# Kernel optimization log

Hardware: AMD Instinct MI355X
Metric: run time of the kernel (lower is better)

Reference implementation:

```python
import jax, jax.numpy as jnp
import numpy as np

B, T, F, U = 64, 512, 256, 1024


def setup_inputs() -> dict:
    key = jax.random.key(0)
    k1, k2, k3, k4 = jax.random.split(key, 4)
    x = jax.random.normal(k1, (B, T, F), dtype=jnp.float32)
    hidden = jnp.zeros((B, U), dtype=jnp.float32)  # initialize_hidden_state()
    # Keras GRU params (reset_after=True, the default): kernel [F,3U], recurrent
    # kernel [U,3U], and two bias vectors (input-side and recurrent-side) [2,3U].
    glorot_k = float(np.sqrt(2.0 / (F + 3 * U)))
    glorot_r = float(np.sqrt(2.0 / (U + 3 * U)))
    kernel = jax.random.normal(k2, (F, 3 * U), dtype=jnp.float32) * glorot_k
    recurrent_kernel = jax.random.normal(k3, (U, 3 * U), dtype=jnp.float32) * glorot_r
    bias = jax.random.normal(k4, (2, 3 * U), dtype=jnp.float32) * 0.02
    return {"x": x, "hidden": hidden, "kernel": kernel,
            "recurrent_kernel": recurrent_kernel, "bias": bias}


def reference(x, hidden, kernel, recurrent_kernel, bias):
    # Keras GRU, reset_after=True, activation=tanh, recurrent_activation=sigmoid.
    # Dropout/recurrent_dropout are inference no-ops (eval mode).
    b_in, b_rec = bias[0], bias[1]
    # Precompute the input projection for all timesteps: [B,T,3U]
    xp = jnp.einsum('btf,fg->btg', x, kernel) + b_in

    def step(h, xt):
        rec = h @ recurrent_kernel + b_rec            # [B,3U]
        xz, xr, xh = jnp.split(xt, 3, axis=-1)
        rz, rr, rh = jnp.split(rec, 3, axis=-1)
        z = jax.nn.sigmoid(xz + rz)                    # update gate
        r = jax.nn.sigmoid(xr + rr)                    # reset gate
        hh = jnp.tanh(xh + r * rh)                     # candidate (reset_after)
        h_new = z * h + (1.0 - z) * hh
        return h_new, h_new

    state, outs = jax.lax.scan(step, hidden, jnp.swapaxes(xp, 0, 1))
    output = jnp.swapaxes(outs, 0, 1)                  # [B,T,U]
    return output, state
```

## Files before the change

### kernel.cpp

```cpp
#include <hip/hip_runtime.h>

#define T_STEPS 512
#define B_ROWS  64
#define F_DIM   256
#define U_DIM   1024
#define G3      3072
#define PACC_BYTES (2 * 12 * 64 * 16)
#define LDS_BYTES (PACC_BYTES + 512)

#define NSLOT  5
#define TILE_B 512
#define GRP_B  (64 * TILE_B)
#define SLOT_B (4 * GRP_B)
#define SENT   0x7FC17FC1u

typedef __bf16 bf16x8 __attribute__((ext_vector_type(8)));
typedef float  f32x4  __attribute__((ext_vector_type(4)));
typedef unsigned int u32x2 __attribute__((ext_vector_type(2)));
typedef unsigned int u32x4 __attribute__((ext_vector_type(4)));

__device__ __forceinline__ float sigmoidf_(float v) {
    return 1.f / (1.f + __expf(-v));
}
__device__ __forceinline__ float tanhf_(float v) {
    float e2 = __expf(2.f * v);
    return 1.f - 2.f / (e2 + 1.f);
}

__global__ __launch_bounds__(256) void transpose_cvt_kernel(
    const float* __restrict__ src, __bf16* __restrict__ dst, int Kdim)
{
    __shared__ float tile[32][33];
    const int n0 = blockIdx.x * 32;
    const int k0 = blockIdx.y * 32;
    const int j  = threadIdx.x & 31;
    const int i0 = threadIdx.x >> 5;
#pragma unroll
    for (int s = 0; s < 4; ++s) {
        int i = i0 * 4 + s;
        tile[i][j] = src[(size_t)(k0 + i) * G3 + n0 + j];
    }
    __syncthreads();
#pragma unroll
    for (int s = 0; s < 4; ++s) {
        int i = i0 * 4 + s;
        dst[(size_t)(n0 + i) * Kdim + k0 + j] = (__bf16)tile[j][i];
    }
}

__global__ __launch_bounds__(256) void init_kernel(
    const float* __restrict__ hidden, char* __restrict__ rot)
{
    const int i = blockIdx.x * 256 + threadIdx.x;
    const int row = i >> 10, u = i & 1023;
    const int rt = row >> 4, rl = row & 15, c = u >> 4, ul = u & 15;
    *(__bf16*)(rot + rt * GRP_B + c * TILE_B + ((rl << 4) + ul) * 2) =
        (__bf16)hidden[i];
    unsigned* s = (unsigned*)(rot + SLOT_B);
    s[2 * i]     = SENT;
    s[2 * i + 1] = SENT;
}

__global__ __launch_bounds__(256, 1) void gru_persistent(
    const float* __restrict__ x,
    const float* __restrict__ hidden,
    const float* __restrict__ bias,
    const float* __restrict__ kern,
    const __bf16* __restrict__ Rt,
    char* __restrict__ rot,
    float* __restrict__ out)
{
    extern __shared__ char lds_raw[];
    float*  pacc  = (float*)lds_raw;
    __bf16* hpack = (__bf16*)(lds_raw + PACC_BYTES);

    const int tid  = threadIdx.x;
    const int lane = tid & 63;
    const int wv   = tid >> 6;
    const int rc   = lane & 15;
    const int kg   = lane >> 4;
    const int bid  = blockIdx.x;
    const int c    = bid & 63;
    const int rt   = bid >> 6;
    const int u    = (c << 4) + rc;
    const int row0 = rt << 4;

    if (wv == 0) __builtin_amdgcn_s_setprio(1);

    const int gu0 = u;
    const int gu1 = U_DIM + u;
    const int gu2 = 2 * U_DIM + u;
    const int xk0 = wv << 6;

    bf16x8 whz[8], whr[8], whh[8];
#pragma unroll
    for (int ki = 0; ki < 8; ++ki) {
        const int col = (wv << 8) + (ki << 5) + (kg << 3);
        whz[ki] = *(const bf16x8*)(Rt + (size_t)gu0 * U_DIM + col);
        whr[ki] = *(const bf16x8*)(Rt + (size_t)gu1 * U_DIM + col);
        whh[ki] = *(const bf16x8*)(Rt + (size_t)gu2 * U_DIM + col);
    }
    bf16x8 wxz[2], wxr[2], wxh[2];
#pragma unroll
    for (int fx = 0; fx < 2; ++fx) {
#pragma unroll
        for (int e = 0; e < 8; ++e) {
            const int k = xk0 + fx * 32 + (kg << 3) + e;
            wxz[fx][e] = (__bf16)kern[(size_t)k * G3 + gu0];
            wxr[fx][e] = (__bf16)kern[(size_t)k * G3 + gu1];
            wxh[fx][e] = (__bf16)kern[(size_t)k * G3 + gu2];
        }
    }

    float hprev[4];
#pragma unroll
    for (int j = 0; j < 4; ++j)
        hprev[j] = hidden[(size_t)(row0 + (kg << 2) + j) * U_DIM + u];

    const float bz_ = bias[u]             + bias[G3 + u];
    const float br_ = bias[U_DIM + u]     + bias[G3 + U_DIM + u];
    const float bhx = bias[2 * U_DIM + u];
    const float bhr = bias[G3 + 2 * U_DIM + u];

    const float* xbase = x + (size_t)(row0 + rc) * (T_STEPS * F_DIM)
                           + xk0 + (kg << 3);

    const int grp_b = rt * GRP_B;
    const int lan_b = (wv << 13) + ((kg >> 1) << 9) + (rc << 5) + ((kg & 1) << 4);
    const int my_b  = grp_b + c * TILE_B + (lane << 3);

    int slot_r = 0, slot_w = 1, slot_p = 3;
    const u32x2 sentv = { SENT, SENT };

    for (int t = 0; t < T_STEPS; ++t) {
        f32x4 accZ  = {0.f, 0.f, 0.f, 0.f};
        f32x4 accR  = {0.f, 0.f, 0.f, 0.f};
        f32x4 accHX = {0.f, 0.f, 0.f, 0.f};
        f32x4 accHR = {0.f, 0.f, 0.f, 0.f};
        const int p = t & 1;

        const char* hb = rot + slot_r * SLOT_B + grp_b + lan_b;
        bf16x8 hfrag[8];
#define HL(ki, m, lit)                                                         \
        asm volatile("global_load_dwordx4 %0, %1, off offset:" lit " sc0 sc1"  \
                     : "=v"(hfrag[ki]) : "v"(hb + (m) * 4096) : "memory");
#define HLOADS()                                                               \
        HL(0,0,"0") HL(1,0,"1024") HL(2,0,"2048") HL(3,0,"3072")               \
        HL(4,1,"0") HL(5,1,"1024") HL(6,1,"2048") HL(7,1,"3072")
        HLOADS()

        const float* ap = xbase + t * F_DIM;
#pragma unroll
        for (int fx = 0; fx < 2; ++fx) {
            const float4 a0 = *(const float4*)(ap + fx * 32);
            const float4 a1 = *(const float4*)(ap + fx * 32 + 4);
            bf16x8 af;
            af[0] = (__bf16)a0.x; af[1] = (__bf16)a0.y;
            af[2] = (__bf16)a0.z; af[3] = (__bf16)a0.w;
            af[4] = (__bf16)a1.x; af[5] = (__bf16)a1.y;
            af[6] = (__bf16)a1.z; af[7] = (__bf16)a1.w;
            accZ  = __builtin_amdgcn_mfma_f32_16x16x32_bf16(af, wxz[fx], accZ,  0, 0, 0);
            accR  = __builtin_amdgcn_mfma_f32_16x16x32_bf16(af, wxr[fx], accR,  0, 0, 0);
            accHX = __builtin_amdgcn_mfma_f32_16x16x32_bf16(af, wxh[fx], accHX, 0, 0, 0);
        }

        if (wv == 0 && t > 0) {
#pragma unroll
            for (int j = 0; j < 4; ++j) {
                const int row = row0 + (kg << 2) + j;
                out[((size_t)row * T_STEPS + (t - 1)) * U_DIM + u] = hprev[j];
            }
        }

        for (;;) {
            asm volatile("s_waitcnt vmcnt(0)" ::: "memory");
            __builtin_amdgcn_sched_barrier(0);
            int ok = 1;
#pragma unroll
            for (int ki = 0; ki < 8; ++ki) {
                const u32x4 w = __builtin_bit_cast(u32x4, hfrag[ki]);
                ok &= (w[0] != SENT) & (w[2] != SENT);
            }
            if (__all(ok)) break;
            HLOADS()
        }
#undef HLOADS
#undef HL

#pragma unroll
        for (int ki = 0; ki < 8; ++ki) {
            const bf16x8 af = hfrag[ki];
            accZ  = __builtin_amdgcn_mfma_f32_16x16x32_bf16(af, whz[ki], accZ,  0, 0, 0);
            accR  = __builtin_amdgcn_mfma_f32_16x16x32_bf16(af, whr[ki], accR,  0, 0, 0);
            accHR = __builtin_amdgcn_mfma_f32_16x16x32_bf16(af, whh[ki], accHR, 0, 0, 0);
        }

        if (wv != 0) {
            const int w1 = wv - 1;
            *(f32x4*)&pacc[(((p * 12) + 0 * 3 + w1) * 64 + lane) * 4] = accZ;
            *(f32x4*)&pacc[(((p * 12) + 1 * 3 + w1) * 64 + lane) * 4] = accR;
            *(f32x4*)&pacc[(((p * 12) + 2 * 3 + w1) * 64 + lane) * 4] = accHX;
            *(f32x4*)&pacc[(((p * 12) + 3 * 3 + w1) * 64 + lane) * 4] = accHR;
        }
        __syncthreads();

        if (wv == 0) {
#pragma unroll
            for (int w1 = 0; w1 < 3; ++w1) {
                accZ  += *(const f32x4*)&pacc[(((p * 12) + 0 * 3 + w1) * 64 + lane) * 4];
                accR  += *(const f32x4*)&pacc[(((p * 12) + 1 * 3 + w1) * 64 + lane) * 4];
                accHX += *(const f32x4*)&pacc[(((p * 12) + 2 * 3 + w1) * 64 + lane) * 4];
                accHR += *(const f32x4*)&pacc[(((p * 12) + 3 * 3 + w1) * 64 + lane) * 4];
            }
#pragma unroll
            for (int j = 0; j < 4; ++j) {
                const float z  = sigmoidf_(accZ[j] + bz_);
                const float r  = sigmoidf_(accR[j] + br_);
                const float hh = tanhf_(accHX[j] + bhx + r * (accHR[j] + bhr));
                hprev[j] = z * hprev[j] + (1.f - z) * hh;
            }
#pragma unroll
            for (int j = 0; j < 4; ++j)
                hpack[(((kg << 2) + j) << 4) + rc] = (__bf16)hprev[j];
            const u32x2 hv = *(const u32x2*)(hpack + ((lane >> 2) << 4) + ((lane & 3) << 2));
            asm volatile("global_store_dwordx2 %0, %1, off sc0 sc1"
                         :: "v"(rot + slot_w * SLOT_B + my_b), "v"(hv) : "memory");
            asm volatile("global_store_dwordx2 %0, %1, off sc0 sc1"
                         :: "v"(rot + slot_p * SLOT_B + my_b), "v"(sentv) : "memory");
        }

        if (++slot_r == NSLOT) slot_r = 0;
        if (++slot_w == NSLOT) slot_w = 0;
        if (++slot_p == NSLOT) slot_p = 0;
    }

    if (wv == 0) {
#pragma unroll
        for (int j = 0; j < 4; ++j) {
            const int row = row0 + (kg << 2) + j;
            out[((size_t)row * T_STEPS + (T_STEPS - 1)) * U_DIM + u] = hprev[j];
            out[(size_t)B_ROWS * T_STEPS * U_DIM + (size_t)row * U_DIM + u] = hprev[j];
        }
    }
}

extern "C" void kernel_launch(void* const* d_in, const int* in_sizes, int n_in,
                              void* d_out, int out_size, void* d_ws, size_t ws_size,
                              hipStream_t stream)
{
    const float* x      = (const float*)d_in[0];
    const float* hidden = (const float*)d_in[1];
    const float* kernel = (const float*)d_in[2];
    const float* rker   = (const float*)d_in[3];
    const float* bias   = (const float*)d_in[4];
    float* out = (float*)d_out;

    const size_t rt_el = (size_t)G3 * U_DIM;
    __bf16* Rt = (__bf16*)d_ws;
    char* rot  = (char*)(Rt + rt_el);

    hipLaunchKernelGGL(transpose_cvt_kernel, dim3(G3 / 32, U_DIM / 32), dim3(256),
                       0, stream, rker, Rt, U_DIM);
    hipLaunchKernelGGL(init_kernel, dim3(256), dim3(256), 0, stream, hidden, rot);

    void* kx = (void*)&x;  void* kh = (void*)&hidden; void* kb = (void*)&bias;
    void* kk = (void*)&kernel; void* kR = (void*)&Rt;
    void* kr = (void*)&rot; void* ko = (void*)&out;
    void* args[7] = { kx, kh, kb, kk, kR, kr, ko };

    auto kfn = gru_persistent;
    (void)hipFuncSetAttribute((const void*)kfn,
                              hipFuncAttributeMaxDynamicSharedMemorySize, LDS_BYTES);
    hipError_t ce = hipLaunchCooperativeKernel(kfn, dim3(256), dim3(256), args,
                                               LDS_BYTES, stream);
    if (ce != hipSuccess) {
        hipLaunchKernelGGL(gru_persistent, dim3(256), dim3(256), LDS_BYTES, stream,
                           x, hidden, bias, kernel, Rt, rot, out);
    }
}
```

Before: 1.388 ms.

## Offload input projection from critical wave and move sentinel store to another wave

Wave 0, which runs the gate math and publishes h, no longer does any input-projection MFMAs. Those chunks are redistributed to waves 1-3 as 3, 3 and 2 K-chunks. The sentinel-clear store moves from wave 0 to wave 3, and wave 0 uses a partial vmcnt wait that skips the output stores it just issued. This shortens the per-step serial path on wave 0, the one that gates cross-block propagation, at the cost of uneven work across the other waves.

```diff
diff --git a/kernel.cpp b/kernel.cpp
--- a/kernel.cpp
+++ b/kernel.cpp
@@ -90,7 +90,6 @@
     const int gu0 = u;
     const int gu1 = U_DIM + u;
     const int gu2 = 2 * U_DIM + u;
-    const int xk0 = wv << 6;
 
     bf16x8 whz[8], whr[8], whh[8];
 #pragma unroll
@@ -100,30 +99,35 @@
         whr[ki] = *(const bf16x8*)(Rt + (size_t)gu1 * U_DIM + col);
         whh[ki] = *(const bf16x8*)(Rt + (size_t)gu2 * U_DIM + col);
     }
-    bf16x8 wxz[2], wxr[2], wxh[2];
-#pragma unroll
-    for (int fx = 0; fx < 2; ++fx) {
-#pragma unroll
-        for (int e = 0; e < 8; ++e) {
-            const int k = xk0 + fx * 32 + (kg << 3) + e;
-            wxz[fx][e] = (__bf16)kern[(size_t)k * G3 + gu0];
-            wxr[fx][e] = (__bf16)kern[(size_t)k * G3 + gu1];
-            wxh[fx][e] = (__bf16)kern[(size_t)k * G3 + gu2];
-        }
-    }
-
-    float hprev[4];
-#pragma unroll
-    for (int j = 0; j < 4; ++j)
-        hprev[j] = hidden[(size_t)(row0 + (kg << 2) + j) * U_DIM + u];
-
+
+    const int xnck = (wv == 1 || wv == 2) ? 3 : (wv == 3 ? 2 : 0);
+    const int xoff = (wv == 2) ? 96 : (wv == 3 ? 192 : 0);
+    bf16x8 wxz[3], wxr[3], wxh[3];
+#pragma unroll
+    for (int ci = 0; ci < 3; ++ci) {
+        if (ci < xnck) {
+#pragma unroll
+            for (int e = 0; e < 8; ++e) {
+                const int k = xoff + ci * 32 + (kg << 3) + e;
+                wxz[ci][e] = (__bf16)kern[(size_t)k * G3 + gu0];
+                wxr[ci][e] = (__bf16)kern[(size_t)k * G3 + gu1];
+                wxh[ci][e] = (__bf16)kern[(size_t)k * G3 + gu2];
+            }
+        }
+    }
+
+    float hprev[4] = {0.f, 0.f, 0.f, 0.f};
+    if (wv == 0) {
+#pragma unroll
+        for (int j = 0; j < 4; ++j)
+            hprev[j] = hidden[(size_t)(row0 + (kg << 2) + j) * U_DIM + u];
+    }
     const float bz_ = bias[u]             + bias[G3 + u];
     const float br_ = bias[U_DIM + u]     + bias[G3 + U_DIM + u];
     const float bhx = bias[2 * U_DIM + u];
     const float bhr = bias[G3 + 2 * U_DIM + u];
 
-    const float* xbase = x + (size_t)(row0 + rc) * (T_STEPS * F_DIM)
-                           + xk0 + (kg << 3);
+    const float* xbase = x + (size_t)(row0 + rc) * (T_STEPS * F_DIM) + (kg << 3);
 
     const int grp_b = rt * GRP_B;
     const int lan_b = (wv << 13) + ((kg >> 1) << 9) + (rc << 5) + ((kg & 1) << 4);
@@ -149,40 +153,62 @@
         HL(4,1,"0") HL(5,1,"1024") HL(6,1,"2048") HL(7,1,"3072")
         HLOADS()
 
-        const float* ap = xbase + t * F_DIM;
-#pragma unroll
-        for (int fx = 0; fx < 2; ++fx) {
-            const float4 a0 = *(const float4*)(ap + fx * 32);
-            const float4 a1 = *(const float4*)(ap + fx * 32 + 4);
-            bf16x8 af;
-            af[0] = (__bf16)a0.x; af[1] = (__bf16)a0.y;
-            af[2] = (__bf16)a0.z; af[3] = (__bf16)a0.w;
-            af[4] = (__bf16)a1.x; af[5] = (__bf16)a1.y;
-            af[6] = (__bf16)a1.z; af[7] = (__bf16)a1.w;
-            accZ  = __builtin_amdgcn_mfma_f32_16x16x32_bf16(af, wxz[fx], accZ,  0, 0, 0);
-            accR  = __builtin_amdgcn_mfma_f32_16x16x32_bf16(af, wxr[fx], accR,  0, 0, 0);
-            accHX = __builtin_amdgcn_mfma_f32_16x16x32_bf16(af, wxh[fx], accHX, 0, 0, 0);
-        }
-
-        if (wv == 0 && t > 0) {
-#pragma unroll
-            for (int j = 0; j < 4; ++j) {
-                const int row = row0 + (kg << 2) + j;
-                out[((size_t)row * T_STEPS + (t - 1)) * U_DIM + u] = hprev[j];
-            }
-        }
-
-        for (;;) {
-            asm volatile("s_waitcnt vmcnt(0)" ::: "memory");
-            __builtin_amdgcn_sched_barrier(0);
-            int ok = 1;
-#pragma unroll
-            for (int ki = 0; ki < 8; ++ki) {
-                const u32x4 w = __builtin_bit_cast(u32x4, hfrag[ki]);
-                ok &= (w[0] != SENT) & (w[2] != SENT);
-            }
-            if (__all(ok)) break;
-            HLOADS()
+        if (wv == 0) {
+            if (t > 0) {
+#pragma unroll
+                for (int j = 0; j < 4; ++j) {
+                    const int row = row0 + (kg << 2) + j;
+                    out[((size_t)row * T_STEPS + (t - 1)) * U_DIM + u] = hprev[j];
+                }
+            }
+            bool first = (t > 0);
+            for (;;) {
+                if (first) {
+                    asm volatile("s_waitcnt vmcnt(4)" ::: "memory");
+                    first = false;
+                } else {
+                    asm volatile("s_waitcnt vmcnt(0)" ::: "memory");
+                }
+                __builtin_amdgcn_sched_barrier(0);
+                int ok = 1;
+#pragma unroll
+                for (int ki = 0; ki < 8; ++ki) {
+                    const u32x4 w = __builtin_bit_cast(u32x4, hfrag[ki]);
+                    ok &= (w[0] != SENT) & (w[2] != SENT);
+                }
+                if (__all(ok)) break;
+                HLOADS()
+            }
+        } else {
+            const float* ap = xbase + t * F_DIM;
+#pragma unroll
+            for (int ci = 0; ci < 3; ++ci) {
+                if (ci < xnck) {
+                    const int k0 = xoff + ci * 32;
+                    const float4 a0 = *(const float4*)(ap + k0);
+                    const float4 a1 = *(const float4*)(ap + k0 + 4);
+                    bf16x8 af;
+                    af[0] = (__bf16)a0.x; af[1] = (__bf16)a0.y;
+                    af[2] = (__bf16)a0.z; af[3] = (__bf16)a0.w;
+                    af[4] = (__bf16)a1.x; af[5] = (__bf16)a1.y;
+                    af[6] = (__bf16)a1.z; af[7] = (__bf16)a1.w;
+                    accZ  = __builtin_amdgcn_mfma_f32_16x16x32_bf16(af, wxz[ci], accZ,  0, 0, 0);
+                    accR  = __builtin_amdgcn_mfma_f32_16x16x32_bf16(af, wxr[ci], accR,  0, 0, 0);
+                    accHX = __builtin_amdgcn_mfma_f32_16x16x32_bf16(af, wxh[ci], accHX, 0, 0, 0);
+                }
+            }
+            for (;;) {
+                asm volatile("s_waitcnt vmcnt(0)" ::: "memory");
+                __builtin_amdgcn_sched_barrier(0);
+                int ok = 1;
+#pragma unroll
+                for (int ki = 0; ki < 8; ++ki) {
+                    const u32x4 w = __builtin_bit_cast(u32x4, hfrag[ki]);
+                    ok &= (w[0] != SENT) & (w[2] != SENT);
+                }
+                if (__all(ok)) break;
+                HLOADS()
+            }
         }
 #undef HLOADS
 #undef HL
@@ -204,6 +230,11 @@
         }
         __syncthreads();
 
+        if (wv == 3) {
+            asm volatile("global_store_dwordx2 %0, %1, off sc0 sc1"
+                         :: "v"(rot + slot_p * SLOT_B + my_b), "v"(sentv) : "memory");
+        }
+
         if (wv == 0) {
 #pragma unroll
             for (int w1 = 0; w1 < 3; ++w1) {
@@ -225,8 +256,6 @@
             const u32x2 hv = *(const u32x2*)(hpack + ((lane >> 2) << 4) + ((lane & 3) << 2));
             asm volatile("global_store_dwordx2 %0, %1, off sc0 sc1"
                          :: "v"(rot + slot_w * SLOT_B + my_b), "v"(hv) : "memory");
-            asm volatile("global_store_dwordx2 %0, %1, off sc0 sc1"
-                         :: "v"(rot + slot_p * SLOT_B + my_b), "v"(sentv) : "memory");
         }
 
         if (++slot_r == NSLOT) slot_r = 0;
```

New measurement: 1.540 ms. 1.11x slower.

## Distribute cross-wave reduction and GRU gate epilogue across all four waves

Applied to the files above, without the earlier changes.

Previously wave 0 alone summed the partial accumulators from the other three waves, computed the gates for all 4 rows per lane, and published the new hidden state. Now every wave writes its partials to LDS. After the barrier, each wave reduces and finalises one row per lane, writes its own slice of the hidden-state tile to the rotation buffer, and writes its own output elements. This shortens the serial epilogue on the critical path of each timestep and removes the wave-0 priority boost. The cost is a larger LDS partial buffer and strided scalar LDS reads in the reduction.

```diff
diff --git a/kernel.cpp b/kernel.cpp
--- a/kernel.cpp
+++ b/kernel.cpp
@@ -5,7 +5,7 @@
 #define F_DIM   256
 #define U_DIM   1024
 #define G3      3072
-#define PACC_BYTES (2 * 12 * 64 * 16)
+#define PACC_BYTES (2 * 16 * 64 * 16)
 #define LDS_BYTES (PACC_BYTES + 512)
 
 #define NSLOT  5
@@ -85,8 +85,6 @@
     const int u    = (c << 4) + rc;
     const int row0 = rt << 4;
 
-    if (wv == 0) __builtin_amdgcn_s_setprio(1);
-
     const int gu0 = u;
     const int gu1 = U_DIM + u;
     const int gu2 = 2 * U_DIM + u;
@@ -112,22 +110,22 @@
         }
     }
 
-    float hprev[4];
-#pragma unroll
-    for (int j = 0; j < 4; ++j)
-        hprev[j] = hidden[(size_t)(row0 + (kg << 2) + j) * U_DIM + u];
-
-    const float bz_ = bias[u]             + bias[G3 + u];
-    const float br_ = bias[U_DIM + u]     + bias[G3 + U_DIM + u];
-    const float bhx = bias[2 * U_DIM + u];
-    const float bhr = bias[G3 + 2 * U_DIM + u];
+    const int myrow = row0 + (wv << 2) + (lane >> 4);
+    const int myu   = (c << 4) + (lane & 15);
+    float hprev_s = hidden[(size_t)myrow * U_DIM + myu];
+
+    const float bz_ = bias[myu]             + bias[G3 + myu];
+    const float br_ = bias[U_DIM + myu]     + bias[G3 + U_DIM + myu];
+    const float bhx = bias[2 * U_DIM + myu];
+    const float bhr = bias[G3 + 2 * U_DIM + myu];
 
     const float* xbase = x + (size_t)(row0 + rc) * (T_STEPS * F_DIM)
                            + xk0 + (kg << 3);
 
     const int grp_b = rt * GRP_B;
     const int lan_b = (wv << 13) + ((kg >> 1) << 9) + (rc << 5) + ((kg & 1) << 4);
-    const int my_b  = grp_b + c * TILE_B + (lane << 3);
+    const int my_b  = grp_b + c * TILE_B + (wv << 7) + ((lane & 15) << 3);
+    __bf16* mypack = hpack + (wv << 6);
 
     int slot_r = 0, slot_w = 1, slot_p = 3;
     const u32x2 sentv = { SENT, SENT };
@@ -164,13 +162,8 @@
             accHX = __builtin_amdgcn_mfma_f32_16x16x32_bf16(af, wxh[fx], accHX, 0, 0, 0);
         }
 
-        if (wv == 0 && t > 0) {
-#pragma unroll
-            for (int j = 0; j < 4; ++j) {
-                const int row = row0 + (kg << 2) + j;
-                out[((size_t)row * T_STEPS + (t - 1)) * U_DIM + u] = hprev[j];
-            }
-        }
+        if (t > 0)
+            out[((size_t)myrow * T_STEPS + (t - 1)) * U_DIM + myu] = hprev_s;
 
         for (;;) {
             asm volatile("s_waitcnt vmcnt(0)" ::: "memory");
@@ -195,38 +188,40 @@
             accHR = __builtin_amdgcn_mfma_f32_16x16x32_bf16(af, whh[ki], accHR, 0, 0, 0);
         }
 
-        if (wv != 0) {
-            const int w1 = wv - 1;
-            *(f32x4*)&pacc[(((p * 12) + 0 * 3 + w1) * 64 + lane) * 4] = accZ;
-            *(f32x4*)&pacc[(((p * 12) + 1 * 3 + w1) * 64 + lane) * 4] = accR;
-            *(f32x4*)&pacc[(((p * 12) + 2 * 3 + w1) * 64 + lane) * 4] = accHX;
-            *(f32x4*)&pacc[(((p * 12) + 3 * 3 + w1) * 64 + lane) * 4] = accHR;
+        {
+            float* dbase = pacc + ((p * 4 + wv) * 4) * 256;
+            *(f32x4*)&dbase[(0 * 64 + lane) * 4] = accZ;
+            *(f32x4*)&dbase[(1 * 64 + lane) * 4] = accR;
+            *(f32x4*)&dbase[(2 * 64 + lane) * 4] = accHX;
+            *(f32x4*)&dbase[(3 * 64 + lane) * 4] = accHR;
         }
         __syncthreads();
 
-        if (wv == 0) {
-#pragma unroll
-            for (int w1 = 0; w1 < 3; ++w1) {
-                accZ  += *(const f32x4*)&pacc[(((p * 12) + 0 * 3 + w1) * 64 + lane) * 4];
-                accR  += *(const f32x4*)&pacc[(((p * 12) + 1 * 3 + w1) * 64 + lane) * 4];
-                accHX += *(const f32x4*)&pacc[(((p * 12) + 2 * 3 + w1) * 64 + lane) * 4];
-                accHR += *(const f32x4*)&pacc[(((p * 12) + 3 * 3 + w1) * 64 + lane) * 4];
+        {
+            const int src = (wv << 4) + (lane & 15);
+            const int jj  = lane >> 4;
+            float vZ = 0.f, vR = 0.f, vHX = 0.f, vHR = 0.f;
+#pragma unroll
+            for (int sv = 0; sv < 4; ++sv) {
+                const float* rb = pacc + ((p * 4 + sv) * 4) * 256;
+                vZ  += rb[(0 * 64 + src) * 4 + jj];
+                vR  += rb[(1 * 64 + src) * 4 + jj];
+                vHX += rb[(2 * 64 + src) * 4 + jj];
+                vHR += rb[(3 * 64 + src) * 4 + jj];
             }
-#pragma unroll
-            for (int j = 0; j < 4; ++j) {
-                const float z  = sigmoidf_(accZ[j] + bz_);
-                const float r  = sigmoidf_(accR[j] + br_);
-                const float hh = tanhf_(accHX[j] + bhx + r * (accHR[j] + bhr));
-                hprev[j] = z * hprev[j] + (1.f - z) * hh;
+            const float z  = sigmoidf_(vZ + bz_);
+            const float r  = sigmoidf_(vR + br_);
+            const float hh = tanhf_(vHX + bhx + r * (vHR + bhr));
+            hprev_s = z * hprev_s + (1.f - z) * hh;
+
+            mypack[((lane >> 4) << 4) + (lane & 15)] = (__bf16)hprev_s;
+            if (lane < 16) {
+                const u32x2 hv = *(const u32x2*)(mypack + (lane << 2));
+                asm volatile("global_store_dwordx2 %0, %1, off sc0 sc1"
+                             :: "v"(rot + slot_w * SLOT_B + my_b), "v"(hv) : "memory");
+                asm volatile("global_store_dwordx2 %0, %1, off sc0 sc1"
+                             :: "v"(rot + slot_p * SLOT_B + my_b), "v"(sentv) : "memory");
             }
-#pragma unroll
-            for (int j = 0; j < 4; ++j)
-                hpack[(((kg << 2) + j) << 4) + rc] = (__bf16)hprev[j];
-            const u32x2 hv = *(const u32x2*)(hpack + ((lane >> 2) << 4) + ((lane & 3) << 2));
-            asm volatile("global_store_dwordx2 %0, %1, off sc0 sc1"
-                         :: "v"(rot + slot_w * SLOT_B + my_b), "v"(hv) : "memory");
-            asm volatile("global_store_dwordx2 %0, %1, off sc0 sc1"
-                         :: "v"(rot + slot_p * SLOT_B + my_b), "v"(sentv) : "memory");
         }
 
         if (++slot_r == NSLOT) slot_r = 0;
@@ -234,14 +229,8 @@
         if (++slot_p == NSLOT) slot_p = 0;
     }
 
-    if (wv == 0) {
-#pragma unroll
-        for (int j = 0; j < 4; ++j) {
-            const int row = row0 + (kg << 2) + j;
-            out[((size_t)row * T_STEPS + (T_STEPS - 1)) * U_DIM + u] = hprev[j];
-            out[(size_t)B_ROWS * T_STEPS * U_DIM + (size_t)row * U_DIM + u] = hprev[j];
-        }
-    }
+    out[((size_t)myrow * T_STEPS + (T_STEPS - 1)) * U_DIM + myu] = hprev_s;
+    out[(size_t)B_ROWS * T_STEPS * U_DIM + (size_t)myrow * U_DIM + myu] = hprev_s;
 }
 
 extern "C" void kernel_launch(void* const* d_in, const int* in_sizes, int n_in,
```

Result: slower. 1.537 ms (+10.7%).
